# Kernel tuning notes

Hardware: AMD Instinct MI355X
Metric: run time of the kernel (lower is better)

Reference implementation:

```python
import jax, jax.numpy as jnp
import numpy as np

L = 7
LVL = 3
B = 8
R = 16
N = 4 ** L  # 16384
P = N // 4  # number of local blocks
T = 4 * R   # ConvLocal output features


def build_permutation_indices(L, l):
    delta = 4 ** (L - l - 1)
    tmp = np.tile(np.arange(4) * delta, delta)
    tmp += np.repeat(np.arange(delta), 4)
    tmp = np.tile(tmp, 4 ** l)
    tmp += np.repeat(np.arange(4 ** l) * 4 ** (L - l), 4 ** (L - l))
    return jnp.asarray(tmp, dtype=jnp.int32)


def setup_inputs() -> dict:
    key = jax.random.key(0)
    kx, k1, k2, k3, k4 = jax.random.split(key, 5)
    scale = 1.0 / np.sqrt(T)
    x = jax.random.normal(kx, (B, 2, N, R), dtype=jnp.float32)
    # flax ConvLocal kernels: (out_spatial, kernel_size*in_features, features)
    W_rr = jax.random.normal(k1, (P, 4 * R, T), dtype=jnp.float32) * scale
    W_ri = jax.random.normal(k2, (P, 4 * R, T), dtype=jnp.float32) * scale
    W_ir = jax.random.normal(k3, (P, 4 * R, T), dtype=jnp.float32) * scale
    W_ii = jax.random.normal(k4, (P, 4 * R, T), dtype=jnp.float32) * scale
    perm_idx = build_permutation_indices(L, LVL)
    return {"x": x, "W_rr": W_rr, "W_ri": W_ri, "W_ir": W_ir,
            "W_ii": W_ii, "perm_idx": perm_idx}


def reference(x, W_rr, W_ri, W_ir, W_ii, perm_idx):
    b, _, n, r = x.shape
    p = n // 4
    # butterfly permutation gather along the spatial axis
    xp = jnp.take(x, perm_idx, axis=2)            # [B, 2, n, r]
    # group into length-4 windows; flax ConvLocal flattens (kernel, in_feat)
    xr = xp[:, 0].reshape(b, p, 4 * r)            # [B, p, 4r]
    xi = xp[:, 1].reshape(b, p, 4 * r)
    # block-diagonal (locally connected) matmuls, complex-style combine
    y_re = jnp.einsum('bpi,pio->bpo', xr, W_rr) + jnp.einsum('bpi,pio->bpo', xi, W_ri)
    y_im = jnp.einsum('bpi,pio->bpo', xr, W_ir) + jnp.einsum('bpi,pio->bpo', xi, W_ii)
    y = jnp.stack([y_re, y_im], axis=1)           # [B, 2, p, 4r]
    return y.reshape(b, 2, n, r)
```

## Files before the change

kernel.cpp:

```cpp
#include <hip/hip_runtime.h>

#define C_N 16384
#define C_R 16
#define C_P 4096
#define C_B 8

__global__ __launch_bounds__(256, 4)
void butterfly_local_conv(const float* __restrict__ x,
                          const float* __restrict__ Wrr,
                          const float* __restrict__ Wri,
                          const float* __restrict__ Wir,
                          const float* __restrict__ Wii,
                          const int*   __restrict__ perm,
                          float* __restrict__ out)
{
    __shared__ float xs[4][2][C_B][64];

    const int t    = threadIdx.x;
    const int w    = t >> 6;
    const int lane = t & 63;
    const int p    = blockIdx.x * 4 + w;

    {
        const int sc = lane >> 5;
        const int sb = (lane >> 2) & 7;
        const int ss = lane & 3;
        const int n  = perm[4 * p + ss];
        const float4* xsrc = (const float4*)(x + (((size_t)(sb * 2 + sc)) * C_N + n) * C_R);
        const float4 v0 = xsrc[0], v1 = xsrc[1], v2 = xsrc[2], v3 = xsrc[3];
        float4* dst = (float4*)(&xs[w][sc][sb][ss * 16]);
        dst[0] = v0; dst[1] = v1; dst[2] = v2; dst[3] = v3;
    }

    const size_t wbase = (size_t)p * 64 * 64 + lane;
    const float* __restrict__ prr = Wrr + wbase;
    const float* __restrict__ pri = Wri + wbase;
    const float* __restrict__ pir = Wir + wbase;
    const float* __restrict__ pii = Wii + wbase;

    float acc_re[C_B], acc_im[C_B];
    #pragma unroll
    for (int b = 0; b < C_B; ++b) { acc_re[b] = 0.0f; acc_im[b] = 0.0f; }

    float bufA[32], bufB[32];

    auto load_chunk = [&](float (&buf)[32], int i0) __attribute__((always_inline)) {
        #pragma unroll
        for (int k = 0; k < 8; ++k) {
            buf[k]      = prr[(i0 + k) * 64];
            buf[8 + k]  = pri[(i0 + k) * 64];
            buf[16 + k] = pir[(i0 + k) * 64];
            buf[24 + k] = pii[(i0 + k) * 64];
        }
    };
    auto compute_chunk = [&](float (&buf)[32], int i0) __attribute__((always_inline)) {
        #pragma unroll
        for (int b = 0; b < C_B; ++b) {
            float xr[8], xi[8];
            *(float4*)&xr[0] = *(const float4*)(&xs[w][0][b][i0]);
            *(float4*)&xr[4] = *(const float4*)(&xs[w][0][b][i0 + 4]);
            *(float4*)&xi[0] = *(const float4*)(&xs[w][1][b][i0]);
            *(float4*)&xi[4] = *(const float4*)(&xs[w][1][b][i0 + 4]);
            #pragma unroll
            for (int k = 0; k < 8; ++k) {
                acc_re[b] = fmaf(xr[k], buf[k],      acc_re[b]);
                acc_re[b] = fmaf(xi[k], buf[8 + k],  acc_re[b]);
                acc_im[b] = fmaf(xr[k], buf[16 + k], acc_im[b]);
                acc_im[b] = fmaf(xi[k], buf[24 + k], acc_im[b]);
            }
        }
    };

    load_chunk(bufA, 0);
    #pragma unroll
    for (int cp = 0; cp < 4; ++cp) {
        load_chunk(bufB, cp * 16 + 8);
        compute_chunk(bufA, cp * 16);
        if (cp < 3) load_chunk(bufA, cp * 16 + 16);
        compute_chunk(bufB, cp * 16 + 8);
    }

    const size_t obase = (size_t)p * 64 + lane;
    #pragma unroll
    for (int b = 0; b < C_B; ++b) {
        out[((size_t)(b * 2 + 0)) * (C_N * C_R) + obase] = acc_re[b];
        out[((size_t)(b * 2 + 1)) * (C_N * C_R) + obase] = acc_im[b];
    }
}

extern "C" void kernel_launch(void* const* d_in, const int* in_sizes, int n_in,
                              void* d_out, int out_size, void* d_ws, size_t ws_size,
                              hipStream_t stream) {
    const float* x    = (const float*)d_in[0];
    const float* Wrr  = (const float*)d_in[1];
    const float* Wri  = (const float*)d_in[2];
    const float* Wir  = (const float*)d_in[3];
    const float* Wii  = (const float*)d_in[4];
    const int*   perm = (const int*)d_in[5];
    float* out = (float*)d_out;

    butterfly_local_conv<<<dim3(C_P / 4), dim3(256), 0, stream>>>(
        x, Wrr, Wri, Wir, Wii, perm, out);
}
```

Before: 270.4 us.

## Split each block into re/im wave tasks with float4 weight loads and shuffle reduction

Each wave now handles one (block, real-or-imag) pair, doubling the grid. The 64 lanes split the input dimension into 4 row groups, and each lane loads float4 weight columns from two matrices in a 3-stage register pipeline. Partial sums are reduced across row groups with xor shuffles, and 16 lanes write float4 outputs. Shared memory rows are padded to 65 floats to avoid bank conflicts. In exchange, x is gathered twice per block, shuffle reductions add work, and 48 of 64 lanes sit idle during the store.

```diff
diff --git a/kernel.cpp b/kernel.cpp
--- a/kernel.cpp
+++ b/kernel.cpp
@@ -4,6 +4,7 @@
 #define C_R 16
 #define C_P 4096
 #define C_B 8
+#define XROW 65
 
 __global__ __launch_bounds__(256, 4)
 void butterfly_local_conv(const float* __restrict__ x,
@@ -14,77 +15,106 @@
                           const int*   __restrict__ perm,
                           float* __restrict__ out)
 {
-    __shared__ float xs[4][2][C_B][64];
+    __shared__ float xs[4][2][C_B][XROW];
 
     const int t    = threadIdx.x;
     const int w    = t >> 6;
-    const int lane = t & 63;
-    const int p    = blockIdx.x * 4 + w;
+    const int l    = t & 63;
+    const int task = blockIdx.x * 4 + w;
+    const int p    = task >> 1;
+    const int comp = task & 1;
+
+    const int sc = l >> 5;
+    const int sb = (l >> 2) & 7;
+    const int ss = l & 3;
+    const int n  = perm[4 * p + ss];
+    const float* xsrc = x + (((size_t)(sb * 2 + sc)) * C_N + n) * C_R;
+    const float4 xv0 = *(const float4*)(xsrc);
+    const float4 xv1 = *(const float4*)(xsrc + 4);
+    const float4 xv2 = *(const float4*)(xsrc + 8);
+    const float4 xv3 = *(const float4*)(xsrc + 12);
+
+    const float* __restrict__ WA = comp ? Wir : Wrr;
+    const float* __restrict__ WB = comp ? Wii : Wri;
+    const int rg = l >> 4;
+    const int cq = l & 15;
+    const float4* __restrict__ WA4 =
+        (const float4*)(WA + (size_t)p * 4096 + rg * 64 + cq * 4);
+    const float4* __restrict__ WB4 =
+        (const float4*)(WB + (size_t)p * 4096 + rg * 64 + cq * 4);
+
+    float4 wa0, wb0, wa1, wb1, wa2, wb2;
+
+#define LOADC(S, C) do { wa##S = WA4[(C) * 64]; wb##S = WB4[(C) * 64]; } while (0)
+
+    LOADC(0, 0); LOADC(1, 1); LOADC(2, 2);
 
     {
-        const int sc = lane >> 5;
-        const int sb = (lane >> 2) & 7;
-        const int ss = lane & 3;
-        const int n  = perm[4 * p + ss];
-        const float4* xsrc = (const float4*)(x + (((size_t)(sb * 2 + sc)) * C_N + n) * C_R);
-        const float4 v0 = xsrc[0], v1 = xsrc[1], v2 = xsrc[2], v3 = xsrc[3];
-        float4* dst = (float4*)(&xs[w][sc][sb][ss * 16]);
-        dst[0] = v0; dst[1] = v1; dst[2] = v2; dst[3] = v3;
+        float* dst = &xs[w][sc][sb][ss * 16];
+        *(float4*)(dst)      = xv0;
+        *(float4*)(dst + 4)  = xv1;
+        *(float4*)(dst + 8)  = xv2;
+        *(float4*)(dst + 12) = xv3;
     }
 
-    const size_t wbase = (size_t)p * 64 * 64 + lane;
-    const float* __restrict__ prr = Wrr + wbase;
-    const float* __restrict__ pri = Wri + wbase;
-    const float* __restrict__ pir = Wir + wbase;
-    const float* __restrict__ pii = Wii + wbase;
+    float4 acc[C_B];
+    #pragma unroll
+    for (int b = 0; b < C_B; ++b) acc[b] = make_float4(0.f, 0.f, 0.f, 0.f);
 
-    float acc_re[C_B], acc_im[C_B];
+    const float* xsr = &xs[w][0][0][0];
+
+#define COMPC(S, C) do {                                                   \
+    const int ib = 4 * (C) + rg;                                           \
+    _Pragma("unroll")                                                      \
+    for (int b = 0; b < C_B; ++b) {                                        \
+        const float xr = xsr[b * XROW + ib];                               \
+        const float xi = xsr[C_B * XROW + b * XROW + ib];                  \
+        acc[b].x = fmaf(xr, wa##S.x, acc[b].x);                            \
+        acc[b].y = fmaf(xr, wa##S.y, acc[b].y);                            \
+        acc[b].z = fmaf(xr, wa##S.z, acc[b].z);                            \
+        acc[b].w = fmaf(xr, wa##S.w, acc[b].w);                            \
+        acc[b].x = fmaf(xi, wb##S.x, acc[b].x);                            \
+        acc[b].y = fmaf(xi, wb##S.y, acc[b].y);                            \
+        acc[b].z = fmaf(xi, wb##S.z, acc[b].z);                            \
+        acc[b].w = fmaf(xi, wb##S.w, acc[b].w);                            \
+    }                                                                      \
+} while (0)
+
+    COMPC(0,  0); LOADC(0,  3);
+    COMPC(1,  1); LOADC(1,  4);
+    COMPC(2,  2); LOADC(2,  5);
+    COMPC(0,  3); LOADC(0,  6);
+    COMPC(1,  4); LOADC(1,  7);
+    COMPC(2,  5); LOADC(2,  8);
+    COMPC(0,  6); LOADC(0,  9);
+    COMPC(1,  7); LOADC(1, 10);
+    COMPC(2,  8); LOADC(2, 11);
+    COMPC(0,  9); LOADC(0, 12);
+    COMPC(1, 10); LOADC(1, 13);
+    COMPC(2, 11); LOADC(2, 14);
+    COMPC(0, 12); LOADC(0, 15);
+    COMPC(1, 13);
+    COMPC(2, 14);
+    COMPC(0, 15);
+
     #pragma unroll
-    for (int b = 0; b < C_B; ++b) { acc_re[b] = 0.0f; acc_im[b] = 0.0f; }
+    for (int b = 0; b < C_B; ++b) {
+        acc[b].x += __shfl_xor(acc[b].x, 16);
+        acc[b].y += __shfl_xor(acc[b].y, 16);
+        acc[b].z += __shfl_xor(acc[b].z, 16);
+        acc[b].w += __shfl_xor(acc[b].w, 16);
+        acc[b].x += __shfl_xor(acc[b].x, 32);
+        acc[b].y += __shfl_xor(acc[b].y, 32);
+        acc[b].z += __shfl_xor(acc[b].z, 32);
+        acc[b].w += __shfl_xor(acc[b].w, 32);
+    }
 
-    float bufA[32], bufB[32];
-
-    auto load_chunk = [&](float (&buf)[32], int i0) __attribute__((always_inline)) {
-        #pragma unroll
-        for (int k = 0; k < 8; ++k) {
-            buf[k]      = prr[(i0 + k) * 64];
-            buf[8 + k]  = pri[(i0 + k) * 64];
-            buf[16 + k] = pir[(i0 + k) * 64];
-            buf[24 + k] = pii[(i0 + k) * 64];
-        }
-    };
-    auto compute_chunk = [&](float (&buf)[32], int i0) __attribute__((always_inline)) {
+    if (l < 16) {
         #pragma unroll
         for (int b = 0; b < C_B; ++b) {
-            float xr[8], xi[8];
-            *(float4*)&xr[0] = *(const float4*)(&xs[w][0][b][i0]);
-            *(float4*)&xr[4] = *(const float4*)(&xs[w][0][b][i0 + 4]);
-            *(float4*)&xi[0] = *(const float4*)(&xs[w][1][b][i0]);
-            *(float4*)&xi[4] = *(const float4*)(&xs[w][1][b][i0 + 4]);
-            #pragma unroll
-            for (int k = 0; k < 8; ++k) {
-                acc_re[b] = fmaf(xr[k], buf[k],      acc_re[b]);
-                acc_re[b] = fmaf(xi[k], buf[8 + k],  acc_re[b]);
-                acc_im[b] = fmaf(xr[k], buf[16 + k], acc_im[b]);
-                acc_im[b] = fmaf(xi[k], buf[24 + k], acc_im[b]);
-            }
+            *(float4*)(out + ((size_t)(b * 2 + comp)) * (C_N * C_R)
+                           + (size_t)p * 64 + l * 4) = acc[b];
         }
-    };
-
-    load_chunk(bufA, 0);
-    #pragma unroll
-    for (int cp = 0; cp < 4; ++cp) {
-        load_chunk(bufB, cp * 16 + 8);
-        compute_chunk(bufA, cp * 16);
-        if (cp < 3) load_chunk(bufA, cp * 16 + 16);
-        compute_chunk(bufB, cp * 16 + 8);
-    }
-
-    const size_t obase = (size_t)p * 64 + lane;
-    #pragma unroll
-    for (int b = 0; b < C_B; ++b) {
-        out[((size_t)(b * 2 + 0)) * (C_N * C_R) + obase] = acc_re[b];
-        out[((size_t)(b * 2 + 1)) * (C_N * C_R) + obase] = acc_im[b];
     }
 }
 
@@ -99,6 +129,6 @@
     const int*   perm = (const int*)d_in[5];
     float* out = (float*)d_out;
 
-    butterfly_local_conv<<<dim3(C_P / 4), dim3(256), 0, stream>>>(
+    butterfly_local_conv<<<dim3(C_P * 2 / 4), dim3(256), 0, stream>>>(
         x, Wrr, Wri, Wir, Wii, perm, out);
 }
```

Measured after the change: 265.0 us. 2.0% less time.
